# Kernel tuning notes

Measured on AMD Instinct MI355X. Metric: run time of the kernel, lower is better.

Reference implementation:

```python
import jax, jax.numpy as jnp
import numpy as np

D_MODEL = 768
N_HEADS = 12
D_K = D_MODEL // N_HEADS

def setup_inputs() -> dict:
    key = jax.random.key(0)
    ks = jax.random.split(key, 9)
    B, S = 4, 2048
    s = 1.0 / np.sqrt(D_MODEL)
    return {
        "x": jax.random.normal(ks[0], (B, S, D_MODEL), dtype=jnp.float32),
        "Wq": jax.random.normal(ks[1], (D_MODEL, D_MODEL), dtype=jnp.float32) * s,
        "bq": jnp.zeros((D_MODEL,), dtype=jnp.float32),
        "Wk": jax.random.normal(ks[2], (D_MODEL, D_MODEL), dtype=jnp.float32) * s,
        "bk": jnp.zeros((D_MODEL,), dtype=jnp.float32),
        "Wv": jax.random.normal(ks[3], (D_MODEL, D_MODEL), dtype=jnp.float32) * s,
        "bv": jnp.zeros((D_MODEL,), dtype=jnp.float32),
        "Wo": jax.random.normal(ks[4], (D_MODEL, D_MODEL), dtype=jnp.float32) * s,
        "bo": jnp.zeros((D_MODEL,), dtype=jnp.float32),
    }

def reference(x, Wq, bq, Wk, bk, Wv, bv, Wo, bo):
    B, S, _ = x.shape
    # projections (nn.Linear: x @ W^T + b; here weights stored as (in, out) so x @ W + b)
    q = x @ Wq + bq
    k = x @ Wk + bk
    v = x @ Wv + bv
    # split heads -> (B, H, S, d_k)
    q = q.reshape(B, S, N_HEADS, D_K).transpose(0, 2, 1, 3)
    k = k.reshape(B, S, N_HEADS, D_K).transpose(0, 2, 1, 3)
    v = v.reshape(B, S, N_HEADS, D_K).transpose(0, 2, 1, 3)
    scores = jnp.einsum('bhqd,bhkd->bhqk', q, k) / jnp.sqrt(jnp.float32(D_K))
    causal = jnp.tril(jnp.ones((S, S), dtype=bool))  # True = keep
    scores = jnp.where(causal, scores, jnp.finfo(scores.dtype).min)
    weights = jax.nn.softmax(scores, axis=-1)  # dropout is identity in eval
    out = jnp.einsum('bhqk,bhkd->bhqd', weights, v)
    out = out.transpose(0, 2, 1, 3).reshape(B, S, D_MODEL)
    return out @ Wo + bo
```

## Files before the change

### kernel.cpp

```cpp
#include <hip/hip_runtime.h>
#include <hip/hip_bf16.h>

#define DM    768
#define HEADS 12
#define DK    64
#define SEQ   2048
#define BATCH 4
#define NE    ((size_t)BATCH * SEQ * DM)
#define KT    12
#define BRICK 8192

typedef short v8s __attribute__((ext_vector_type(8)));
typedef float v4f __attribute__((ext_vector_type(4)));

#define LDS_PTR(p) ((__attribute__((address_space(3))) unsigned int*)(p))
#define GLB_PTR(p) ((const __attribute__((address_space(1))) unsigned int*)(p))

__device__ __forceinline__ unsigned short f2bf(float f) {
    union { float f; unsigned u; } v; v.f = f;
    unsigned r = (v.u + 0x7FFFu + ((v.u >> 16) & 1u)) >> 16;
    return (unsigned short)r;
}
__device__ __forceinline__ unsigned pk2(float a, float b) {
    union { float f; unsigned u; } x, y; x.f = a; y.f = b;
    return (x.u >> 16) | (y.u & 0xFFFF0000u);
}
__device__ __forceinline__ unsigned pk2r(float a, float b) {
    return (unsigned)f2bf(a) | ((unsigned)f2bf(b) << 16);
}
__device__ __forceinline__ float fexp2(float x) {
#if __has_builtin(__builtin_amdgcn_exp2f)
    return __builtin_amdgcn_exp2f(x);
#else
    return __expf(x * 0.69314718056f);
#endif
}

#define QSCALE 0.18033688011112042f

__global__ __launch_bounds__(256)
void cvt_x_kernel(const float* __restrict__ x, unsigned short* __restrict__ xb) {
    const size_t p = ((size_t)blockIdx.x * 256 + threadIdx.x) * 8;
    const int m = (int)(p / DM);
    const int k = (int)(p % DM);
    const float4 a = *(const float4*)(x + p);
    const float4 b = *(const float4*)(x + p + 4);
    v8s o;
    o[0] = (short)f2bf(a.x); o[1] = (short)f2bf(a.y);
    o[2] = (short)f2bf(a.z); o[3] = (short)f2bf(a.w);
    o[4] = (short)f2bf(b.x); o[5] = (short)f2bf(b.y);
    o[6] = (short)f2bf(b.z); o[7] = (short)f2bf(b.w);
    const size_t dst = ((size_t)(m >> 7) * KT + (k >> 6)) * BRICK + (size_t)(m & 127) * 64 + (k & 63);
    *(v8s*)(xb + dst) = o;
}

__global__ __launch_bounds__(256)
void cvt_w_kernel(const float* __restrict__ W0, const float* __restrict__ W1,
                  const float* __restrict__ W2, const float* __restrict__ W3,
                  unsigned short* __restrict__ wt) {
    __shared__ unsigned short T[64][72];
    const int z = blockIdx.z;
    const float* W = (z == 0) ? W0 : (z == 1) ? W1 : (z == 2) ? W2 : W3;
    const float scale = (z == 0) ? QSCALE : 1.0f;
    const int k0 = blockIdx.x * 64, n0 = blockIdx.y * 64;
    const int t = threadIdx.x;
    {
        const int kr = t >> 2;
        const int ns = (t & 3) * 16;
        #pragma unroll
        for (int j = 0; j < 4; ++j) {
            const float4 v = *(const float4*)(W + (size_t)(k0 + kr) * DM + n0 + ns + j * 4);
            T[ns + j * 4 + 0][kr] = f2bf(v.x * scale);
            T[ns + j * 4 + 1][kr] = f2bf(v.y * scale);
            T[ns + j * 4 + 2][kr] = f2bf(v.z * scale);
            T[ns + j * 4 + 3][kr] = f2bf(v.w * scale);
        }
    }
    __syncthreads();
    {
        unsigned short* dst = wt + (size_t)z * DM * DM +
            ((size_t)(n0 >> 7) * KT + (k0 >> 6)) * BRICK + (size_t)(n0 & 64) * 64;
        const int n = t >> 2;
        const int ks = (t & 3) * 16;
        #pragma unroll
        for (int j = 0; j < 2; ++j)
            *(v8s*)(dst + (size_t)n * 64 + ks + j * 8) = *(const v8s*)&T[n][ks + j * 8];
    }
}

__global__ __launch_bounds__(256)
void gemm_qkv_kernel(const unsigned short* __restrict__ xb, const unsigned short* __restrict__ wtbuf,
                     const float* __restrict__ bq, const float* __restrict__ bk,
                     const float* __restrict__ bv,
                     unsigned short* __restrict__ qb, unsigned short* __restrict__ kb,
                     unsigned short* __restrict__ vtb) {
    __shared__ unsigned short smem[32768];
    const int idx = blockIdx.x;
    const int xcd = idx & 7, g = idx >> 3;
    const int mb = xcd + 8 * (g & 7);
    const int yb = g >> 3;
    const int z = yb / 6;
    const int N0 = (yb % 6) * 128;
    const float* bias = (z == 0) ? bq : (z == 1) ? bk : bv;
    const float bscale = (z == 0) ? QSCALE : 1.0f;

    const int t = threadIdx.x;
    const int w = t >> 6, lane = t & 63, quad = lane >> 4, l15 = lane & 15;
    const int wm = w >> 1, wn = w & 1;
    const int M0 = mb * 128;

    const unsigned short* gA = xb + (size_t)mb * (KT * BRICK);
    const unsigned short* gB = wtbuf + (size_t)yb * (KT * BRICK);

    const int r8 = lane >> 3;
    const int c8 = (lane & 7) ^ r8;
    const int goff = r8 * 64 + c8 * 8;
    const int rl = l15 & 7, rh = l15 >> 3;

    v4f acc[4][4];
    #pragma unroll
    for (int i = 0; i < 4; ++i)
        #pragma unroll
        for (int j = 0; j < 4; ++j) acc[i][j] = (v4f){0, 0, 0, 0};

    #pragma unroll
    for (int u = 0; u < 4; ++u) {
        const int win = w * 4 + u;
        __builtin_amdgcn_global_load_lds(GLB_PTR(gA + win * 512 + goff), LDS_PTR(smem + win * 512), 16, 0, 0);
        __builtin_amdgcn_global_load_lds(GLB_PTR(gB + win * 512 + goff), LDS_PTR(smem + 16384 + win * 512), 16, 0, 0);
    }
    __syncthreads();

    for (int kt = 0; kt < KT; ++kt) {
        const int cur = kt & 1;
        if (kt + 1 < KT) {
            const unsigned short* ta = gA + (kt + 1) * BRICK;
            const unsigned short* tb = gB + (kt + 1) * BRICK;
            const int nb = (1 - cur) * 8192;
            #pragma unroll
            for (int u = 0; u < 4; ++u) {
                const int win = w * 4 + u;
                __builtin_amdgcn_global_load_lds(GLB_PTR(ta + win * 512 + goff), LDS_PTR(smem + nb + win * 512), 16, 0, 0);
                __builtin_amdgcn_global_load_lds(GLB_PTR(tb + win * 512 + goff), LDS_PTR(smem + 16384 + nb + win * 512), 16, 0, 0);
            }
        }
        const unsigned short* As = smem + cur * 8192;
        const unsigned short* Bs = smem + 16384 + cur * 8192;
        #pragma unroll
        for (int kc = 0; kc < 2; ++kc) {
            const int cs = ((kc << 2) | quad) ^ rl;
            v8s a[4], b[4];
            #pragma unroll
            for (int i = 0; i < 4; ++i)
                a[i] = *(const v8s*)&As[(wm * 8 + i * 2 + rh) * 512 + rl * 64 + cs * 8];
            #pragma unroll
            for (int j = 0; j < 4; ++j)
                b[j] = *(const v8s*)&Bs[(wn * 8 + j * 2 + rh) * 512 + rl * 64 + cs * 8];
            #pragma unroll
            for (int i = 0; i < 4; ++i)
                #pragma unroll
                for (int j = 0; j < 4; ++j)
                    acc[i][j] = __builtin_amdgcn_mfma_f32_16x16x32_bf16(a[i], b[j], acc[i][j], 0, 0, 0);
        }
        __syncthreads();
    }

    const int b_ = M0 >> 11;
    const int sidx0 = M0 & 2047;
    const int h0 = N0 >> 6;

    if (z < 2) {
        unsigned short* outp = (z == 0) ? qb : kb;
        #pragma unroll
        for (int j = 0; j < 4; ++j) {
            const int n = N0 + wn * 64 + j * 16 + l15;
            const int h = n >> 6, d = n & 63;
            const float bv_ = bias[n] * bscale;
            #pragma unroll
            for (int i = 0; i < 4; ++i)
                #pragma unroll
                for (int r = 0; r < 4; ++r) {
                    const int sidx = sidx0 + wm * 64 + i * 16 + quad * 4 + r;
                    outp[(((size_t)(b_ * HEADS + h) * SEQ + sidx) << 6) + d] = f2bf(acc[i][j][r] + bv_);
                }
        }
    } else {
        unsigned short* Ts = smem;
        #pragma unroll
        for (int p = 0; p < 2; ++p) {
            __syncthreads();
            if (wm == p) {
                #pragma unroll
                for (int j = 0; j < 4; ++j) {
                    const int dloc = wn * 64 + j * 16 + l15;
                    const float bv_ = bias[N0 + dloc];
                    #pragma unroll
                    for (int i = 0; i < 4; ++i)
                        #pragma unroll
                        for (int r = 0; r < 4; ++r)
                            Ts[dloc * 72 + i * 16 + quad * 4 + r] = f2bf(acc[i][j][r] + bv_);
                }
            }
            __syncthreads();
            const int dloc = t >> 1, ms = (t & 1) * 32;
            const int h = h0 + (dloc >> 6), d = dloc & 63;
            unsigned short* dst = vtb + (((size_t)(b_ * HEADS + h) * DK + d) << 11) + sidx0 + p * 64 + ms;
            #pragma unroll
            for (int jj = 0; jj < 4; ++jj)
                *(v8s*)(dst + jj * 8) = *(const v8s*)&Ts[dloc * 72 + ms + jj * 8];
        }
    }
}

__global__ __launch_bounds__(256)
void gemm_out_kernel(const unsigned short* __restrict__ ob, const unsigned short* __restrict__ wto,
                     const float* __restrict__ bias, float* __restrict__ out) {
    __shared__ unsigned short smem[32768];
    const int idx = blockIdx.x;
    const int xcd = idx & 7, g = idx >> 3;
    const int mb = xcd + 8 * (g & 7);
    const int nb = g >> 3;
    const int t = threadIdx.x;
    const int w = t >> 6, lane = t & 63, quad = lane >> 4, l15 = lane & 15;
    const int wm = w >> 1, wn = w & 1;
    const int M0 = mb * 128;
    const int N0 = nb * 128;

    const unsigned short* gA = ob + (size_t)mb * (KT * BRICK);
    const unsigned short* gB = wto + (size_t)nb * (KT * BRICK);

    const int r8 = lane >> 3;
    const int c8 = (lane & 7) ^ r8;
    const int goff = r8 * 64 + c8 * 8;
    const int rl = l15 & 7, rh = l15 >> 3;

    v4f acc[4][4];
    #pragma unroll
    for (int i = 0; i < 4; ++i)
        #pragma unroll
        for (int j = 0; j < 4; ++j) acc[i][j] = (v4f){0, 0, 0, 0};

    #pragma unroll
    for (int u = 0; u < 4; ++u) {
        const int win = w * 4 + u;
        __builtin_amdgcn_global_load_lds(GLB_PTR(gA + win * 512 + goff), LDS_PTR(smem + win * 512), 16, 0, 0);
        __builtin_amdgcn_global_load_lds(GLB_PTR(gB + win * 512 + goff), LDS_PTR(smem + 16384 + win * 512), 16, 0, 0);
    }
    __syncthreads();

    for (int kt = 0; kt < KT; ++kt) {
        const int cur = kt & 1;
        if (kt + 1 < KT) {
            const unsigned short* ta = gA + (kt + 1) * BRICK;
            const unsigned short* tb = gB + (kt + 1) * BRICK;
            const int nxt = (1 - cur) * 8192;
            #pragma unroll
            for (int u = 0; u < 4; ++u) {
                const int win = w * 4 + u;
                __builtin_amdgcn_global_load_lds(GLB_PTR(ta + win * 512 + goff), LDS_PTR(smem + nxt + win * 512), 16, 0, 0);
                __builtin_amdgcn_global_load_lds(GLB_PTR(tb + win * 512 + goff), LDS_PTR(smem + 16384 + nxt + win * 512), 16, 0, 0);
            }
        }
        const unsigned short* As = smem + cur * 8192;
        const unsigned short* Bs = smem + 16384 + cur * 8192;
        #pragma unroll
        for (int kc = 0; kc < 2; ++kc) {
            const int cs = ((kc << 2) | quad) ^ rl;
            v8s a[4], b[4];
            #pragma unroll
            for (int i = 0; i < 4; ++i)
                a[i] = *(const v8s*)&As[(wm * 8 + i * 2 + rh) * 512 + rl * 64 + cs * 8];
            #pragma unroll
            for (int j = 0; j < 4; ++j)
                b[j] = *(const v8s*)&Bs[(wn * 8 + j * 2 + rh) * 512 + rl * 64 + cs * 8];
            #pragma unroll
            for (int i = 0; i < 4; ++i)
                #pragma unroll
                for (int j = 0; j < 4; ++j)
                    acc[i][j] = __builtin_amdgcn_mfma_f32_16x16x32_bf16(a[i], b[j], acc[i][j], 0, 0, 0);
        }
        __syncthreads();
    }

    #pragma unroll
    for (int j = 0; j < 4; ++j) {
        const int n = N0 + wn * 64 + j * 16 + l15;
        const float bv_ = bias[n];
        #pragma unroll
        for (int i = 0; i < 4; ++i)
            #pragma unroll
            for (int r = 0; r < 4; ++r) {
                const int m = M0 + wm * 64 + i * 16 + quad * 4 + r;
                out[(size_t)m * DM + n] = acc[i][j][r] + bv_;
            }
    }
}

__global__ __launch_bounds__(256, 4)
void attn_kernel(const unsigned short* __restrict__ Q, const unsigned short* __restrict__ K,
                 const unsigned short* __restrict__ VT, unsigned short* __restrict__ O) {
    __shared__ unsigned short Kb[2][64][64];
    __shared__ unsigned short Vb[2][64][64];
    __shared__ unsigned short Ps[4][16][64];
    const int t = threadIdx.x;
    const int w = t >> 6, lane = t & 63, quad = lane >> 4, l15 = lane & 15;
    const int e7 = l15 & 7;

    const int idx = blockIdx.x;
    const int xcd = idx & 7;
    const int g   = idx >> 3;
    const int bh  = xcd + 8 * (g % 6);
    const int s   = 31 - g / 6;
    const int q0  = s * 64;
    const int nkt = s + 1;
    const size_t kvbase = (size_t)bh * SEQ * DK;

    v8s qf[2];
    #pragma unroll
    for (int c = 0; c < 2; ++c)
        qf[c] = *(const v8s*)(Q + kvbase + (size_t)(q0 + w * 16 + l15) * DK + c * 32 + quad * 8);

    v4f o[4];
    #pragma unroll
    for (int nf = 0; nf < 4; ++nf) o[nf] = (v4f){0, 0, 0, 0};
    v4f os = (v4f){0, 0, 0, 0};
    const v4f zero4 = (v4f){0, 0, 0, 0};

    const short one_bf = (short)0x3F80;
    const v8s ones = (v8s){one_bf, one_bf, one_bf, one_bf, one_bf, one_bf, one_bf, one_bf};

    const int srow = t >> 3;
    const int sc16 = t & 7;
    const int scolsw = (sc16 ^ (srow & 7)) * 8;
    const int gcol = sc16 * 8;

    v8s kr0 = *(const v8s*)(K  + kvbase + (size_t)srow * DK + gcol);
    v8s kr1 = *(const v8s*)(K  + kvbase + (size_t)(srow + 32) * DK + gcol);
    v8s vr0 = *(const v8s*)(VT + kvbase + ((size_t)srow << 11) + gcol);
    v8s vr1 = *(const v8s*)(VT + kvbase + ((size_t)(srow + 32) << 11) + gcol);
    *(v8s*)&Kb[0][srow][scolsw]      = kr0;
    *(v8s*)&Kb[0][srow + 32][scolsw] = kr1;
    *(v8s*)&Vb[0][srow][scolsw]      = vr0;
    *(v8s*)&Vb[0][srow + 32][scolsw] = vr1;
    __syncthreads();

    const int q_ = q0 + w * 16 + l15;

    for (int kt = 0; kt < nkt; ++kt) {
        const int k0 = kt * 64;
        const int cur = kt & 1;
        if (kt + 1 < nkt) {
            const int kn = k0 + 64;
            kr0 = *(const v8s*)(K  + kvbase + (size_t)(kn + srow) * DK + gcol);
            kr1 = *(const v8s*)(K  + kvbase + (size_t)(kn + srow + 32) * DK + gcol);
            vr0 = *(const v8s*)(VT + kvbase + ((size_t)srow << 11) + kn + gcol);
            vr1 = *(const v8s*)(VT + kvbase + ((size_t)(srow + 32) << 11) + kn + gcol);
        }

        v4f sc[4];
        #pragma unroll
        for (int s4 = 0; s4 < 4; ++s4) {
            const v8s kf = *(const v8s*)&Kb[cur][s4 * 16 + l15][(quad ^ e7) * 8];
            sc[s4] = __builtin_amdgcn_mfma_f32_16x16x32_bf16(kf, qf[0], zero4, 0, 0, 0);
        }
        #pragma unroll
        for (int s4 = 0; s4 < 4; ++s4) {
            const v8s kf = *(const v8s*)&Kb[cur][s4 * 16 + l15][((4 | quad) ^ e7) * 8];
            sc[s4] = __builtin_amdgcn_mfma_f32_16x16x32_bf16(kf, qf[1], sc[s4], 0, 0, 0);
        }

        {
            const bool msk = (kt == s);
            #pragma unroll
            for (int s4 = 0; s4 < 4; ++s4) {
                float p[4];
                #pragma unroll
                for (int r = 0; r < 4; ++r) p[r] = fexp2(sc[s4][r]);
                if (msk) {
                    #pragma unroll
                    for (int r = 0; r < 4; ++r) {
                        const int key = k0 + s4 * 16 + quad * 4 + r;
                        if (key > q_) p[r] = 0.f;
                    }
                }
                uint2 pkv; pkv.x = pk2(p[0], p[1]); pkv.y = pk2(p[2], p[3]);
                const int col8 = (s4 * 4 + quad) ^ (e7 << 1);
                *(uint2*)&Ps[w][l15][col8 * 4] = pkv;
            }
        }

        #pragma unroll
        for (int kc = 0; kc < 2; ++kc) {
            const int c16 = ((kc * 4 + quad) ^ e7) * 8;
            const v8s pf = *(const v8s*)&Ps[w][l15][c16];
            os = __builtin_amdgcn_mfma_f32_16x16x32_bf16(ones, pf, os, 0, 0, 0);
            #pragma unroll
            for (int nf = 0; nf < 4; ++nf) {
                const v8s vf = *(const v8s*)&Vb[cur][nf * 16 + l15][c16];
                o[nf] = __builtin_amdgcn_mfma_f32_16x16x32_bf16(vf, pf, o[nf], 0, 0, 0);
            }
        }

        if (kt + 1 < nkt) {
            const int nxt = 1 - cur;
            *(v8s*)&Kb[nxt][srow][scolsw]      = kr0;
            *(v8s*)&Kb[nxt][srow + 32][scolsw] = kr1;
            *(v8s*)&Vb[nxt][srow][scolsw]      = vr0;
            *(v8s*)&Vb[nxt][srow + 32][scolsw] = vr1;
        }
        __syncthreads();
    }

    const float inv = 1.f / os[0];

    const int b = bh / HEADS, h = bh % HEADS;
    const size_t br = ((size_t)(b * 16 + (q0 >> 7)) * KT + h) * BRICK;
    const int rowl = (q0 & 127) + w * 16 + l15;
    #pragma unroll
    for (int nf = 0; nf < 4; ++nf) {
        uint2 a2;
        a2.x = pk2r(o[nf][0] * inv, o[nf][1] * inv);
        a2.y = pk2r(o[nf][2] * inv, o[nf][3] * inv);
        *(uint2*)(O + br + (size_t)rowl * 64 + nf * 16 + quad * 4) = a2;
    }
}

extern "C" void kernel_launch(void* const* d_in, const int* in_sizes, int n_in,
                              void* d_out, int out_size, void* d_ws, size_t ws_size,
                              hipStream_t stream) {
    const float* x  = (const float*)d_in[0];
    const float* Wq = (const float*)d_in[1];
    const float* bq = (const float*)d_in[2];
    const float* Wk = (const float*)d_in[3];
    const float* bk = (const float*)d_in[4];
    const float* Wv = (const float*)d_in[5];
    const float* bv = (const float*)d_in[6];
    const float* Wo = (const float*)d_in[7];
    const float* bo = (const float*)d_in[8];
    float* out = (float*)d_out;

    unsigned short* xb  = (unsigned short*)d_ws;
    unsigned short* qb  = xb  + NE;
    unsigned short* kb  = qb  + NE;
    unsigned short* vtb = kb  + NE;
    unsigned short* wt  = vtb + NE;
    unsigned short* ob  = xb;

    cvt_x_kernel<<<dim3(NE / (8 * 256)), 256, 0, stream>>>(x, xb);
    cvt_w_kernel<<<dim3(12, 12, 4), 256, 0, stream>>>(Wq, Wk, Wv, Wo, wt);
    gemm_qkv_kernel<<<dim3(1152), 256, 0, stream>>>(xb, wt, bq, bk, bv, qb, kb, vtb);
    attn_kernel<<<dim3(1536), 256, 0, stream>>>(qb, kb, vtb, ob);
    gemm_out_kernel<<<dim3(384), 256, 0, stream>>>(ob, wt + (size_t)3 * DM * DM, bo, out);
}
```

Measured before the change: 202.4 us.

## Double attention query tile to 128 rows per block with 8 waves sharing K/V

Each attention block now covers 128 query rows using 8 waves (512 threads) instead of 64 rows with 4 waves, so every K/V tile staged in shared memory serves twice as many queries. The aim is to halve global K/V traffic and the number of blocks. Each thread now loads one K row and one V row instead of two. The trade-off is that waves in the first half of the tile sit idle on the final key tile because of the causal mask. Larger blocks also change the occupancy and launch-bounds constraints.

```diff
diff --git a/kernel.cpp b/kernel.cpp
--- a/kernel.cpp
+++ b/kernel.cpp
@@ -296,23 +296,25 @@
     }
 }
 
-__global__ __launch_bounds__(256, 4)
+__global__ __launch_bounds__(512, 6)
 void attn_kernel(const unsigned short* __restrict__ Q, const unsigned short* __restrict__ K,
                  const unsigned short* __restrict__ VT, unsigned short* __restrict__ O) {
     __shared__ unsigned short Kb[2][64][64];
     __shared__ unsigned short Vb[2][64][64];
-    __shared__ unsigned short Ps[4][16][64];
+    __shared__ unsigned short Ps[8][16][64];
     const int t = threadIdx.x;
     const int w = t >> 6, lane = t & 63, quad = lane >> 4, l15 = lane & 15;
     const int e7 = l15 & 7;
+    const int qh = w >> 2;
 
     const int idx = blockIdx.x;
     const int xcd = idx & 7;
     const int g   = idx >> 3;
     const int bh  = xcd + 8 * (g % 6);
-    const int s   = 31 - g / 6;
-    const int q0  = s * 64;
-    const int nkt = s + 1;
+    const int j   = 15 - g / 6;
+    const int q0  = j * 128;
+    const int nkt = 2 * j + 2;
+    const int lastk = 2 * j + qh;
     const size_t kvbase = (size_t)bh * SEQ * DK;
 
     v8s qf[2];
@@ -334,14 +336,10 @@
     const int scolsw = (sc16 ^ (srow & 7)) * 8;
     const int gcol = sc16 * 8;
 
-    v8s kr0 = *(const v8s*)(K  + kvbase + (size_t)srow * DK + gcol);
-    v8s kr1 = *(const v8s*)(K  + kvbase + (size_t)(srow + 32) * DK + gcol);
-    v8s vr0 = *(const v8s*)(VT + kvbase + ((size_t)srow << 11) + gcol);
-    v8s vr1 = *(const v8s*)(VT + kvbase + ((size_t)(srow + 32) << 11) + gcol);
-    *(v8s*)&Kb[0][srow][scolsw]      = kr0;
-    *(v8s*)&Kb[0][srow + 32][scolsw] = kr1;
-    *(v8s*)&Vb[0][srow][scolsw]      = vr0;
-    *(v8s*)&Vb[0][srow + 32][scolsw] = vr1;
+    v8s kr = *(const v8s*)(K  + kvbase + (size_t)srow * DK + gcol);
+    v8s vr = *(const v8s*)(VT + kvbase + ((size_t)srow << 11) + gcol);
+    *(v8s*)&Kb[0][srow][scolsw] = kr;
+    *(v8s*)&Vb[0][srow][scolsw] = vr;
     __syncthreads();
 
     const int q_ = q0 + w * 16 + l15;
@@ -351,62 +349,60 @@
         const int cur = kt & 1;
         if (kt + 1 < nkt) {
             const int kn = k0 + 64;
-            kr0 = *(const v8s*)(K  + kvbase + (size_t)(kn + srow) * DK + gcol);
-            kr1 = *(const v8s*)(K  + kvbase + (size_t)(kn + srow + 32) * DK + gcol);
-            vr0 = *(const v8s*)(VT + kvbase + ((size_t)srow << 11) + kn + gcol);
-            vr1 = *(const v8s*)(VT + kvbase + ((size_t)(srow + 32) << 11) + kn + gcol);
-        }
-
-        v4f sc[4];
-        #pragma unroll
-        for (int s4 = 0; s4 < 4; ++s4) {
-            const v8s kf = *(const v8s*)&Kb[cur][s4 * 16 + l15][(quad ^ e7) * 8];
-            sc[s4] = __builtin_amdgcn_mfma_f32_16x16x32_bf16(kf, qf[0], zero4, 0, 0, 0);
-        }
-        #pragma unroll
-        for (int s4 = 0; s4 < 4; ++s4) {
-            const v8s kf = *(const v8s*)&Kb[cur][s4 * 16 + l15][((4 | quad) ^ e7) * 8];
-            sc[s4] = __builtin_amdgcn_mfma_f32_16x16x32_bf16(kf, qf[1], sc[s4], 0, 0, 0);
-        }
-
-        {
-            const bool msk = (kt == s);
+            kr = *(const v8s*)(K  + kvbase + (size_t)(kn + srow) * DK + gcol);
+            vr = *(const v8s*)(VT + kvbase + ((size_t)srow << 11) + kn + gcol);
+        }
+
+        if (kt <= lastk) {
+            v4f sc[4];
             #pragma unroll
             for (int s4 = 0; s4 < 4; ++s4) {
-                float p[4];
-                #pragma unroll
-                for (int r = 0; r < 4; ++r) p[r] = fexp2(sc[s4][r]);
-                if (msk) {
+                const v8s kf = *(const v8s*)&Kb[cur][s4 * 16 + l15][(quad ^ e7) * 8];
+                sc[s4] = __builtin_amdgcn_mfma_f32_16x16x32_bf16(kf, qf[0], zero4, 0, 0, 0);
+            }
+            #pragma unroll
+            for (int s4 = 0; s4 < 4; ++s4) {
+                const v8s kf = *(const v8s*)&Kb[cur][s4 * 16 + l15][((4 | quad) ^ e7) * 8];
+                sc[s4] = __builtin_amdgcn_mfma_f32_16x16x32_bf16(kf, qf[1], sc[s4], 0, 0, 0);
+            }
+
+            {
+                const bool msk = (kt == lastk);
+                #pragma unroll
+                for (int s4 = 0; s4 < 4; ++s4) {
+                    float p[4];
                     #pragma unroll
-                    for (int r = 0; r < 4; ++r) {
-                        const int key = k0 + s4 * 16 + quad * 4 + r;
-                        if (key > q_) p[r] = 0.f;
+                    for (int r = 0; r < 4; ++r) p[r] = fexp2(sc[s4][r]);
+                    if (msk) {
+                        #pragma unroll
+                        for (int r = 0; r < 4; ++r) {
+                            const int key = k0 + s4 * 16 + quad * 4 + r;
+                            if (key > q_) p[r] = 0.f;
+                        }
                     }
+                    uint2 pkv; pkv.x = pk2(p[0], p[1]); pkv.y = pk2(p[2], p[3]);
+                    const int col8 = (s4 * 4 + quad) ^ (e7 << 1);
+                    *(uint2*)&Ps[w][l15][col8 * 4] = pkv;
                 }
-                uint2 pkv; pkv.x = pk2(p[0], p[1]); pkv.y = pk2(p[2], p[3]);
-                const int col8 = (s4 * 4 + quad) ^ (e7 << 1);
-                *(uint2*)&Ps[w][l15][col8 * 4] = pkv;
-            }
-        }
-
-        #pragma unroll
-        for (int kc = 0; kc < 2; ++kc) {
-            const int c16 = ((kc * 4 + quad) ^ e7) * 8;
-            const v8s pf = *(const v8s*)&Ps[w][l15][c16];
-            os = __builtin_amdgcn_mfma_f32_16x16x32_bf16(ones, pf, os, 0, 0, 0);
-            #pragma unroll
-            for (int nf = 0; nf < 4; ++nf) {
-                const v8s vf = *(const v8s*)&Vb[cur][nf * 16 + l15][c16];
-                o[nf] = __builtin_amdgcn_mfma_f32_16x16x32_bf16(vf, pf, o[nf], 0, 0, 0);
+            }
+
+            #pragma unroll
+            for (int kc = 0; kc < 2; ++kc) {
+                const int c16 = ((kc * 4 + quad) ^ e7) * 8;
+                const v8s pf = *(const v8s*)&Ps[w][l15][c16];
+                os = __builtin_amdgcn_mfma_f32_16x16x32_bf16(ones, pf, os, 0, 0, 0);
+                #pragma unroll
+                for (int nf = 0; nf < 4; ++nf) {
+                    const v8s vf = *(const v8s*)&Vb[cur][nf * 16 + l15][c16];
+                    o[nf] = __builtin_amdgcn_mfma_f32_16x16x32_bf16(vf, pf, o[nf], 0, 0, 0);
+                }
             }
         }
 
         if (kt + 1 < nkt) {
             const int nxt = 1 - cur;
-            *(v8s*)&Kb[nxt][srow][scolsw]      = kr0;
-            *(v8s*)&Kb[nxt][srow + 32][scolsw] = kr1;
-            *(v8s*)&Vb[nxt][srow][scolsw]      = vr0;
-            *(v8s*)&Vb[nxt][srow + 32][scolsw] = vr1;
+            *(v8s*)&Kb[nxt][srow][scolsw] = kr;
+            *(v8s*)&Vb[nxt][srow][scolsw] = vr;
         }
         __syncthreads();
     }
@@ -414,8 +410,8 @@
     const float inv = 1.f / os[0];
 
     const int b = bh / HEADS, h = bh % HEADS;
-    const size_t br = ((size_t)(b * 16 + (q0 >> 7)) * KT + h) * BRICK;
-    const int rowl = (q0 & 127) + w * 16 + l15;
+    const size_t br = ((size_t)(b * 16 + j) * KT + h) * BRICK;
+    const int rowl = w * 16 + l15;
     #pragma unroll
     for (int nf = 0; nf < 4; ++nf) {
         uint2 a2;
@@ -449,6 +445,6 @@
     cvt_x_kernel<<<dim3(NE / (8 * 256)), 256, 0, stream>>>(x, xb);
     cvt_w_kernel<<<dim3(12, 12, 4), 256, 0, stream>>>(Wq, Wk, Wv, Wo, wt);
     gemm_qkv_kernel<<<dim3(1152), 256, 0, stream>>>(xb, wt, bq, bk, bv, qb, kb, vtb);
-    attn_kernel<<<dim3(1536), 256, 0, stream>>>(qb, kb, vtb, ob);
+    attn_kernel<<<dim3(768), 512, 0, stream>>>(qb, kb, vtb, ob);
     gemm_out_kernel<<<dim3(384), 256, 0, stream>>>(ob, wt + (size_t)3 * DM * DM, bo, out);
 }
```

Measured after the change: 217.6 us. 1.08x slower.
